# Performance work log

Measured on AMD Instinct MI355X. Metric: run time of the kernel, lower is better.

The kernel has to match this reference:

```python
import jax, jax.numpy as jnp
import numpy as np

DOF = 4
NUM_ITER = 10
Z_MIN = 0.1
EPS = 1e-5
MIN_LM_DIAG = 1e-6
MAX_LM_DIAG = 1e32
MIN_REL_DECREASE = 1e-3
INIT_RADIUS = 30.0
MAX_RADIUS = 1e16


def _proj_single(pose, x3d, K):
    # pose: (4,) [x, y, z, yaw]; x3d: (N,3); K: (3,3) -> (N,2)
    yaw = pose[3]
    s, c = jnp.sin(yaw), jnp.cos(yaw)
    z = jnp.zeros_like(c)
    o = jnp.ones_like(c)
    R = jnp.stack([jnp.stack([c, z, s]),
                   jnp.stack([z, o, z]),
                   jnp.stack([-s, z, c])])  # yaw_to_rot_mat
    p = x3d @ R.T + pose[:3]                 # (N,3) camera-frame points
    ph = p @ K.T                              # (N,3)
    zc = jnp.maximum(ph[:, 2:3], Z_MIN)       # depth clamp
    return ph[:, :2] / zc


def _res_single(pose, x3d, x2d, w2d, K):
    # weighted reprojection residual, flattened to (2N,)
    return ((_proj_single(pose, x3d, K) - x2d) * w2d).reshape(-1)


_res_b = jax.vmap(_res_single)
_jac_b = jax.vmap(jax.jacfwd(_res_single))  # (B, 2N, 4)


def _cost(r):
    return 0.5 * jnp.sum(r * r, axis=-1)


def lm_solve(x3d, x2d, w2d, pose_init, cam_mats):
    B = pose_init.shape[0]
    dt = pose_init.dtype
    pose = pose_init
    residual = _res_b(pose, x3d, x2d, w2d, cam_mats)
    jac = _jac_b(pose, x3d, x2d, w2d, cam_mats)
    cost = _cost(residual)
    radius = jnp.full((B,), INIT_RADIUS, dt)
    dec = jnp.full((B,), 2.0, dt)
    eye = jnp.eye(DOF, dtype=dt)

    def body(carry, _):
        pose, jac, residual, cost, radius, dec = carry
        jtj = jnp.einsum('bri,brj->bij', jac, jac)
        diag = jnp.clip(jnp.diagonal(jtj, axis1=-2, axis2=-1), MIN_LM_DIAG, MAX_LM_DIAG)
        jtj_lm = jtj + (diag / radius[:, None])[:, :, None] * eye  # LM damping
        grad = jnp.einsum('bri,br->bi', jac, residual)
        step = -jnp.linalg.solve(jtj_lm, grad[..., None])[..., 0]   # (B,4)
        pose_new = pose + step
        residual_new = _res_b(pose_new, x3d, x2d, w2d, cam_mats)
        cost_new = _cost(residual_new)
        jac_new = _jac_b(pose_new, x3d, x2d, w2d, cam_mats)
        # trust-region step acceptance (Ceres-style)
        model_cost_change = -jnp.einsum('bi,bi->b', step,
                                        grad + 0.5 * jnp.einsum('bij,bj->bi', jtj, step))
        rel = (cost - cost_new) / model_cost_change
        success = (rel >= MIN_REL_DECREASE) & (model_cost_change > 0.0)
        radius_s = jnp.minimum(radius / jnp.maximum(1.0 - (2.0 * rel - 1.0) ** 3, 1.0 / 3.0),
                               MAX_RADIUS)
        radius = jnp.where(success, radius_s, radius / dec)
        dec = jnp.where(success, 2.0, dec * 2.0)
        m = success[:, None]
        pose = jnp.where(m, pose_new, pose)
        residual = jnp.where(m, residual_new, residual)
        jac = jnp.where(success[:, None, None], jac_new, jac)
        cost = jnp.where(success, cost_new, cost)
        return (pose, jac, residual, cost, radius, dec), None

    (pose, jac, residual, cost, radius, dec), _ = jax.lax.scan(
        body, (pose, jac, residual, cost, radius, dec), None, length=NUM_ITER)
    return pose, cost


def gn_step(x3d, x2d, w2d, pose, cam_mats):
    residual = _res_b(pose, x3d, x2d, w2d, cam_mats)
    jac = _jac_b(pose, x3d, x2d, w2d, cam_mats)
    jtj = jnp.einsum('bri,brj->bij', jac, jac) + EPS * jnp.eye(DOF, dtype=pose.dtype)
    grad = jnp.einsum('bri,br->bi', jac, residual)
    return -jnp.linalg.solve(jtj, grad[..., None])[..., 0]


def setup_inputs() -> dict:
    key = jax.random.key(0)
    k1, k2, k3, k4, k5, k6 = jax.random.split(key, 6)
    B, N = 4096, 512
    x3d = jax.random.normal(k1, (B, N, 3), jnp.float32) * 0.5
    yaw_gt = jax.random.uniform(k2, (B, 1), jnp.float32, -0.5, 0.5)
    txy = jax.random.normal(k3, (B, 2), jnp.float32) * 0.2
    pose_gt = jnp.concatenate([txy, jnp.full((B, 1), 6.0, jnp.float32), yaw_gt], axis=-1)
    K = jnp.broadcast_to(jnp.array([[500.0, 0.0, 256.0],
                                    [0.0, 500.0, 256.0],
                                    [0.0, 0.0, 1.0]], jnp.float32), (B, 3, 3))
    x2d = jax.vmap(_proj_single)(pose_gt, x3d, K) + jax.random.normal(k4, (B, N, 2), jnp.float32) * 2.0
    w2d = jax.random.uniform(k5, (B, N, 2), jnp.float32) * 0.02
    noise = jax.random.normal(k6, (B, 4), jnp.float32) * jnp.array([0.2, 0.2, 0.5, 0.2], jnp.float32)
    pose_init = pose_gt + noise
    return {'x3d': x3d, 'x2d': x2d, 'w2d': w2d, 'pose_init': pose_init, 'cam_mats': K}


def reference(x3d, x2d, w2d, pose_init, cam_mats):
    # LMSolver.forward with with_pose_opt_plus=True, with_cost=True
    pose_opt, cost = lm_solve(x3d, x2d, w2d, pose_init, cam_mats)
    pose_opt_plus = pose_opt + gn_step(x3d, x2d, w2d, pose_opt, cam_mats)
    return pose_opt, cost, pose_opt_plus
```

## Files before the change

kernel.cpp:

```cpp
#include <hip/hip_runtime.h>
#include <math.h>

#define NUM_ITER 10
#define Z_MIN 0.1f

typedef float v2f __attribute__((ext_vector_type(2)));

__device__ inline float uniform_f(float v) {
    return __int_as_float(__builtin_amdgcn_readfirstlane(__float_as_int(v)));
}

__device__ inline float fast_rcp(float x) {
    return __builtin_amdgcn_rcpf(x);
}

__device__ inline v2f fma2(v2f a, v2f b, v2f c) {
#if __has_builtin(__builtin_elementwise_fma)
    return __builtin_elementwise_fma(a, b, c);
#else
    v2f r; r.x = fmaf(a.x, b.x, c.x); r.y = fmaf(a.y, b.y, c.y); return r;
#endif
}

__device__ inline v2f max2(v2f a, v2f b) {
#if __has_builtin(__builtin_elementwise_max)
    return __builtin_elementwise_max(a, b);
#else
    v2f r; r.x = fmaxf(a.x, b.x); r.y = fmaxf(a.y, b.y); return r;
#endif
}

template <int M>
__device__ inline void wave_reduce_uniform(float (&a)[M]) {
#pragma unroll
    for (int k = 0; k < M; ++k) {
        int t = __builtin_amdgcn_update_dpp(0, __float_as_int(a[k]), 0x121, 0xf, 0xf, true);
        a[k] += __int_as_float(t);
    }
#pragma unroll
    for (int k = 0; k < M; ++k) {
        int t = __builtin_amdgcn_update_dpp(0, __float_as_int(a[k]), 0x122, 0xf, 0xf, true);
        a[k] += __int_as_float(t);
    }
#pragma unroll
    for (int k = 0; k < M; ++k) {
        int t = __builtin_amdgcn_update_dpp(0, __float_as_int(a[k]), 0x124, 0xf, 0xf, true);
        a[k] += __int_as_float(t);
    }
#pragma unroll
    for (int k = 0; k < M; ++k) {
        int t = __builtin_amdgcn_update_dpp(0, __float_as_int(a[k]), 0x128, 0xf, 0xf, true);
        a[k] += __int_as_float(t);
    }
#pragma unroll
    for (int k = 0; k < M; ++k) {
        int t = __builtin_amdgcn_update_dpp(0, __float_as_int(a[k]), 0x142, 0xf, 0xf, true);
        a[k] += __int_as_float(t);
    }
#pragma unroll
    for (int k = 0; k < M; ++k) {
        int t = __builtin_amdgcn_update_dpp(0, __float_as_int(a[k]), 0x143, 0xf, 0xf, true);
        a[k] += __int_as_float(t);
    }
#pragma unroll
    for (int k = 0; k < M; ++k) {
        a[k] = __int_as_float(__builtin_amdgcn_readlane(__float_as_int(a[k]), 63));
    }
}

__device__ inline void solve4_spd(const float t[10], const float b[4], float x[4]) {
    const float d0 = t[0];
    const float i0 = fast_rcp(d0);
    const float L10 = t[1] * i0, L20 = t[2] * i0, L30 = t[3] * i0;
    const float d1 = t[4] - L10 * t[1];
    const float i1 = fast_rcp(d1);
    const float L21 = (t[5] - L20 * t[1]) * i1;
    const float L31 = (t[6] - L30 * t[1]) * i1;
    const float d2 = t[7] - L20 * t[2] - L21 * L21 * d1;
    const float i2 = fast_rcp(d2);
    const float L32 = (t[8] - L30 * t[2] - L31 * L21 * d1) * i2;
    const float d3 = t[9] - L30 * t[3] - L31 * L31 * d1 - L32 * L32 * d2;
    const float i3 = fast_rcp(d3);
    const float y0 = b[0];
    const float y1 = b[1] - L10 * y0;
    const float y2 = b[2] - L20 * y0 - L21 * y1;
    const float y3 = b[3] - L30 * y0 - L31 * y1 - L32 * y2;
    const float z0 = y0 * i0, z1 = y1 * i1, z2 = y2 * i2, z3 = y3 * i3;
    x[3] = z3;
    x[2] = z2 - L32 * z3;
    x[1] = z1 - L21 * x[2] - L31 * x[3];
    x[0] = z0 - L10 * x[1] - L20 * x[2] - L30 * x[3];
}

template <int PPL, bool EXACT>
__global__ __launch_bounds__(256) void lm_kernel(
    const float* __restrict__ x3d, const float* __restrict__ x2d,
    const float* __restrict__ w2d, const float* __restrict__ pose_init,
    const float* __restrict__ K, float* __restrict__ out, int B, int N)
{
    static_assert(PPL % 2 == 0, "PPL must be even");
    constexpr int NP = PPL / 2;

    const int wave = threadIdx.x >> 6;
    const int lane = threadIdx.x & 63;
    const int item = blockIdx.x * 4 + wave;
    if (item >= B) return;

    const float* Kb = K + (size_t)item * 9;
    const float K00 = uniform_f(Kb[0]), K01 = uniform_f(Kb[1]), K02 = uniform_f(Kb[2]);
    const float K10 = uniform_f(Kb[3]), K11 = uniform_f(Kb[4]), K12 = uniform_f(Kb[5]);
    const float K20 = uniform_f(Kb[6]), K21 = uniform_f(Kb[7]), K22 = uniform_f(Kb[8]);
    const bool spec = (K01 == 0.f) && (K10 == 0.f) && (K20 == 0.f) &&
                      (K21 == 0.f) && (K22 == 1.f);
    const float cxfx = K02 * fast_rcp(K00);
    const float cyfy = K12 * fast_rcp(K11);

    v2f X2[NP], Y2[NP], Z2[NP], Au2[NP], Av2[NP], Bu2[NP], Bv2[NP];
    if (EXACT) {
        const float4* p3 = reinterpret_cast<const float4*>(x3d + (size_t)item * N * 3) + lane * (3 * PPL / 4);
        const float4* p2 = reinterpret_cast<const float4*>(x2d + (size_t)item * N * 2) + lane * (2 * PPL / 4);
        const float4* pw = reinterpret_cast<const float4*>(w2d + (size_t)item * N * 2) + lane * (2 * PPL / 4);
        float f3[3 * PPL];
#pragma unroll
        for (int i = 0; i < 3 * PPL / 4; ++i) {
            const float4 t = p3[i];
            f3[4 * i] = t.x; f3[4 * i + 1] = t.y; f3[4 * i + 2] = t.z; f3[4 * i + 3] = t.w;
        }
#pragma unroll
        for (int j = 0; j < NP; ++j) {
            X2[j].x = f3[6 * j];     X2[j].y = f3[6 * j + 3];
            Y2[j].x = f3[6 * j + 1]; Y2[j].y = f3[6 * j + 4];
            Z2[j].x = f3[6 * j + 2]; Z2[j].y = f3[6 * j + 5];
        }
#pragma unroll
        for (int j = 0; j < NP; ++j) {
            const float4 tw = pw[j];
            const float4 to = p2[j];
            if (spec) {
                Au2[j].x = tw.x * K00;          Au2[j].y = tw.z * K00;
                Av2[j].x = tw.y * K11;          Av2[j].y = tw.w * K11;
                Bu2[j].x = tw.x * (K02 - to.x); Bu2[j].y = tw.z * (K02 - to.z);
                Bv2[j].x = tw.y * (K12 - to.y); Bv2[j].y = tw.w * (K12 - to.w);
            } else {
                Au2[j].x = tw.x;         Au2[j].y = tw.z;
                Av2[j].x = tw.y;         Av2[j].y = tw.w;
                Bu2[j].x = -tw.x * to.x; Bu2[j].y = -tw.z * to.z;
                Bv2[j].x = -tw.y * to.y; Bv2[j].y = -tw.w * to.w;
            }
        }
    } else {
        const float* x3b = x3d + (size_t)item * N * 3;
        const float* x2b = x2d + (size_t)item * N * 2;
        const float* w2b = w2d + (size_t)item * N * 2;
#pragma unroll
        for (int j = 0; j < NP; ++j) {
#pragma unroll
            for (int h = 0; h < 2; ++h) {
                const int p = lane + (2 * j + h) * 64;
                float X = 0.f, Y = 0.f, Z = 0.f, au = 0.f, av = 0.f, bu = 0.f, bv = 0.f;
                if (p < N) {
                    X = x3b[3 * p]; Y = x3b[3 * p + 1]; Z = x3b[3 * p + 2];
                    const float wu = w2b[2 * p], wv = w2b[2 * p + 1];
                    const float uo = x2b[2 * p], vo = x2b[2 * p + 1];
                    if (spec) {
                        au = wu * K00;        av = wv * K11;
                        bu = wu * (K02 - uo); bv = wv * (K12 - vo);
                    } else {
                        au = wu;       av = wv;
                        bu = -wu * uo; bv = -wv * vo;
                    }
                }
                if (h == 0) { X2[j].x = X; Y2[j].x = Y; Z2[j].x = Z;
                              Au2[j].x = au; Av2[j].x = av; Bu2[j].x = bu; Bv2[j].x = bv; }
                else        { X2[j].y = X; Y2[j].y = Y; Z2[j].y = Z;
                              Au2[j].y = au; Av2[j].y = av; Bu2[j].y = bu; Bv2[j].y = bv; }
            }
        }
    }

    float JtJ[10], grad[4];
    float cost = 0.f, radius = 30.0f, dec = 2.0f, mcc = 0.f;
#pragma unroll
    for (int k = 0; k < 10; ++k) JtJ[k] = 0.f;
#pragma unroll
    for (int k = 0; k < 4; ++k) grad[k] = 0.f;

    float ax = pose_init[(size_t)item * 4 + 0];
    float ay = pose_init[(size_t)item * 4 + 1];
    float az = pose_init[(size_t)item * 4 + 2];
    float ayaw = pose_init[(size_t)item * 4 + 3];
    float ex = ax, ey = ay, ez = az, eyaw = ayaw;
    float sn = __sinf(eyaw), cs = __cosf(eyaw);

#pragma clang loop unroll(disable)
    for (int it = 0; it <= NUM_ITER; ++it) {
        float acc[15];

        if (spec) {
            v2f s2[14];
#pragma unroll
            for (int k = 0; k < 14; ++k) s2[k] = (v2f)(0.f);
            const v2f cs2 = (v2f)(cs),  sn2 = (v2f)(sn);
            const v2f ex2 = (v2f)(ex),  ey2 = (v2f)(ey), ez2 = (v2f)(ez);
            const v2f zm2 = (v2f)(Z_MIN);
#pragma unroll
            for (int j = 0; j < NP; ++j) {
                const v2f X = X2[j], Y = Y2[j], Z = Z2[j];
                const v2f px = fma2(cs2, X, fma2(sn2, Z, ex2));
                const v2f py = Y + ey2;
                const v2f pz = fma2(-sn2, X, fma2(cs2, Z, ez2));
                const v2f zc = max2(pz, zm2);
                v2f inv; inv.x = fast_rcp(zc.x); inv.y = fast_rcp(zc.y);
                const v2f alpha = px * inv;
                const v2f beta  = py * inv;
                v2f t, tv;
                t.x  = (pz.x > Z_MIN) ? -alpha.x : cxfx;
                t.y  = (pz.y > Z_MIN) ? -alpha.y : cxfx;
                tv.x = (pz.x > Z_MIN) ? -beta.x  : cyfy;
                tv.y = (pz.y > Z_MIN) ? -beta.y  : cyfy;
                const v2f ru  = fma2(Au2[j], alpha, Bu2[j]);
                const v2f rv  = fma2(Av2[j], beta,  Bv2[j]);
                const v2f Ju0 = Au2[j] * inv;
                const v2f Jv1 = Av2[j] * inv;
                const v2f Ju2 = Ju0 * t;
                const v2f Jv2 = Jv1 * tv;
                const v2f a  = pz - ez2;
                const v2f bb = ex2 - px;
                const v2f q  = fma2(t, bb, a);
                const v2f Ju3 = Ju0 * q;
                const v2f Jv3 = Jv2 * bb;
                s2[0]  = fma2(Ju0, Ju0, s2[0]);
                s2[1]  = fma2(Ju0, Ju2, s2[1]);
                s2[2]  = fma2(Ju0, Ju3, s2[2]);
                s2[3]  = fma2(Jv1, Jv1, s2[3]);
                s2[4]  = fma2(Jv1, Jv2, s2[4]);
                s2[5]  = fma2(Jv1, Jv3, s2[5]);
                s2[6]  = fma2(Ju2, Ju2, fma2(Jv2, Jv2, s2[6]));
                s2[7]  = fma2(Ju2, Ju3, fma2(Jv2, Jv3, s2[7]));
                s2[8]  = fma2(Ju3, Ju3, fma2(Jv3, Jv3, s2[8]));
                s2[9]  = fma2(Ju0, ru, s2[9]);
                s2[10] = fma2(Jv1, rv, s2[10]);
                s2[11] = fma2(Ju2, ru, fma2(Jv2, rv, s2[11]));
                s2[12] = fma2(Ju3, ru, fma2(Jv3, rv, s2[12]));
                s2[13] = fma2(ru, ru, fma2(rv, rv, s2[13]));
            }
            float s[14];
#pragma unroll
            for (int k = 0; k < 14; ++k) s[k] = s2[k].x + s2[k].y;
            wave_reduce_uniform<14>(s);
            acc[0] = s[0];  acc[1] = 0.f;  acc[2] = s[1];  acc[3] = s[2];
            acc[4] = s[3];  acc[5] = s[4]; acc[6] = s[5];  acc[7] = s[6];
            acc[8] = s[7];  acc[9] = s[8];
            acc[10] = s[9]; acc[11] = s[10]; acc[12] = s[11]; acc[13] = s[12];
            acc[14] = s[13];
        } else {
#pragma unroll
            for (int k = 0; k < 15; ++k) acc[k] = 0.f;
#pragma unroll
            for (int j = 0; j < NP; ++j) {
#pragma unroll
                for (int h = 0; h < 2; ++h) {
                    const float X = h ? X2[j].y : X2[j].x;
                    const float Y = h ? Y2[j].y : Y2[j].x;
                    const float Z = h ? Z2[j].y : Z2[j].x;
                    const float au = h ? Au2[j].y : Au2[j].x;
                    const float av = h ? Av2[j].y : Av2[j].x;
                    const float bu = h ? Bu2[j].y : Bu2[j].x;
                    const float bv = h ? Bv2[j].y : Bv2[j].x;
                    const float px = fmaf(cs, X, fmaf(sn, Z, ex));
                    const float py = Y + ey;
                    const float pz = fmaf(-sn, X, fmaf(cs, Z, ez));
                    const float nu = fmaf(K00, px, fmaf(K01, py, K02 * pz));
                    const float nv = fmaf(K10, px, fmaf(K11, py, K12 * pz));
                    const float w  = fmaf(K20, px, fmaf(K21, py, K22 * pz));
                    const float zc  = fmaxf(w, Z_MIN);
                    const float inv = fast_rcp(zc);
                    const float gu = au * inv, gv = av * inv;
                    const float ru = fmaf(nu, gu, bu);
                    const float rv = fmaf(nv, gv, bv);
                    const float u = nu * inv, v = nv * inv;
                    const float fl  = (w > Z_MIN) ? 1.f : 0.f;
                    const float ufl = u * fl, vfl = v * fl;
                    const float a  = pz - ez;
                    const float bb = ex - px;
                    const float dnu3 = fmaf(K00, a, K02 * bb);
                    const float dnv3 = fmaf(K10, a, K12 * bb);
                    const float dw3  = fmaf(K20, a, K22 * bb);
                    float Ju[4], Jv[4];
                    Ju[0] = gu * fmaf(-ufl, K20, K00);  Jv[0] = gv * fmaf(-vfl, K20, K10);
                    Ju[1] = gu * fmaf(-ufl, K21, K01);  Jv[1] = gv * fmaf(-vfl, K21, K11);
                    Ju[2] = gu * fmaf(-ufl, K22, K02);  Jv[2] = gv * fmaf(-vfl, K22, K12);
                    Ju[3] = gu * fmaf(-ufl, dw3, dnu3); Jv[3] = gv * fmaf(-vfl, dw3, dnv3);
                    int idx = 0;
#pragma unroll
                    for (int r = 0; r < 4; ++r)
#pragma unroll
                        for (int c = r; c < 4; ++c) {
                            acc[idx] = fmaf(Ju[r], Ju[c], fmaf(Jv[r], Jv[c], acc[idx]));
                            ++idx;
                        }
#pragma unroll
                    for (int r = 0; r < 4; ++r)
                        acc[10 + r] = fmaf(Ju[r], ru, fmaf(Jv[r], rv, acc[10 + r]));
                    acc[14] = fmaf(ru, ru, fmaf(rv, rv, acc[14]));
                }
            }
            wave_reduce_uniform<15>(acc);
        }

        const float costN = 0.5f * acc[14];

        bool accept;
        if (it == 0) {
            accept = true;
        } else {
            const float rel = (cost - costN) * fast_rcp(mcc);
            const bool success = (rel >= 1e-3f) && (mcc > 0.0f);
            if (success) {
                const float q = 2.0f * rel - 1.0f;
                const float denom = fmaxf(1.0f - q * q * q, 1.0f / 3.0f);
                radius = fminf(radius * fast_rcp(denom), 1e16f);
                dec = 2.0f;
            } else {
                radius = radius * fast_rcp(dec);
                dec = dec * 2.0f;
            }
            accept = success;
        }
        if (accept) {
#pragma unroll
            for (int k = 0; k < 10; ++k) JtJ[k] = acc[k];
#pragma unroll
            for (int k = 0; k < 4; ++k) grad[k] = acc[10 + k];
            cost = costN;
            if (it > 0) { ax = ex; ay = ey; az = ez; ayaw = eyaw; }
        }

        if (it < NUM_ITER) {
            float A[10], rhs[4], stf[4];
#pragma unroll
            for (int k = 0; k < 10; ++k) A[k] = JtJ[k];
            const float irad = fast_rcp(radius);
            const float e0 = fminf(fmaxf(JtJ[0], 1e-6f), 1e32f) * irad;
            const float e1 = fminf(fmaxf(JtJ[4], 1e-6f), 1e32f) * irad;
            const float e2 = fminf(fmaxf(JtJ[7], 1e-6f), 1e32f) * irad;
            const float e3 = fminf(fmaxf(JtJ[9], 1e-6f), 1e32f) * irad;
            A[0] += e0; A[4] += e1; A[7] += e2; A[9] += e3;
#pragma unroll
            for (int r = 0; r < 4; ++r) rhs[r] = -grad[r];
            solve4_spd(A, rhs, stf);
            ex = ax + stf[0]; ey = ay + stf[1]; ez = az + stf[2]; eyaw = ayaw + stf[3];
            const float s0 = stf[0], s1 = stf[1], s2 = stf[2], s3 = stf[3];
            const float sg = s0 * grad[0] + s1 * grad[1] + s2 * grad[2] + s3 * grad[3];
            float sd = e0 * s0 * s0;
            sd = fmaf(e1 * s1, s1, sd);
            sd = fmaf(e2 * s2, s2, sd);
            sd = fmaf(e3 * s3, s3, sd);
            mcc = 0.5f * (sd - sg);
            sn = __sinf(eyaw); cs = __cosf(eyaw);
        } else if (lane == 0) {
            float* out_pose = out;
            float* out_cost = out + (size_t)B * 4;
            float* out_plus = out + (size_t)B * 5;
            out_pose[(size_t)item * 4 + 0] = ax;
            out_pose[(size_t)item * 4 + 1] = ay;
            out_pose[(size_t)item * 4 + 2] = az;
            out_pose[(size_t)item * 4 + 3] = ayaw;
            out_cost[item] = cost;
            float A[10], rhs[4], stf[4];
#pragma unroll
            for (int k = 0; k < 10; ++k) A[k] = JtJ[k];
            A[0] += 1e-5f; A[4] += 1e-5f; A[7] += 1e-5f; A[9] += 1e-5f;
#pragma unroll
            for (int r = 0; r < 4; ++r) rhs[r] = -grad[r];
            solve4_spd(A, rhs, stf);
            out_plus[(size_t)item * 4 + 0] = ax + stf[0];
            out_plus[(size_t)item * 4 + 1] = ay + stf[1];
            out_plus[(size_t)item * 4 + 2] = az + stf[2];
            out_plus[(size_t)item * 4 + 3] = ayaw + stf[3];
        }
    }
}

extern "C" void kernel_launch(void* const* d_in, const int* in_sizes, int n_in,
                              void* d_out, int out_size, void* d_ws, size_t ws_size,
                              hipStream_t stream) {
    const float* x3d       = (const float*)d_in[0];
    const float* x2d       = (const float*)d_in[1];
    const float* w2d       = (const float*)d_in[2];
    const float* pose_init = (const float*)d_in[3];
    const float* cam       = (const float*)d_in[4];
    float* out = (float*)d_out;

    const int B = in_sizes[3] / 4;
    const int N = in_sizes[0] / (3 * B);
    const int grid = (B + 3) / 4;

    if (N == 512) {
        lm_kernel<8, true><<<grid, 256, 0, stream>>>(x3d, x2d, w2d, pose_init, cam, out, B, N);
    } else if (N == 256) {
        lm_kernel<4, true><<<grid, 256, 0, stream>>>(x3d, x2d, w2d, pose_init, cam, out, B, N);
    } else if (N <= 128) {
        lm_kernel<2, false><<<grid, 256, 0, stream>>>(x3d, x2d, w2d, pose_init, cam, out, B, N);
    } else if (N <= 256) {
        lm_kernel<4, false><<<grid, 256, 0, stream>>>(x3d, x2d, w2d, pose_init, cam, out, B, N);
    } else if (N <= 512) {
        lm_kernel<8, false><<<grid, 256, 0, stream>>>(x3d, x2d, w2d, pose_init, cam, out, B, N);
    } else {
        lm_kernel<16, false><<<grid, 256, 0, stream>>>(x3d, x2d, w2d, pose_init, cam, out, B, N);
    }
}
```

Before: 125.8 us.

## Split each batch item across two waves with shared-memory cross-wave reduction

Each LM problem is now handled by two wavefronts instead of one. Each wave processes half of the points and combines its partial JtJ, gradient and cost sums with the other wave through shared memory, using a parity double-buffer and __syncthreads each iteration. This halves the per-lane point work and register footprint and doubles the number of waves, which targets the latency of the serial per-item iteration chain. In exchange it adds block-wide barriers and LDS traffic, duplicates the scalar solve in both waves, and doubles the grid size.

```diff
diff --git a/kernel.cpp b/kernel.cpp
--- a/kernel.cpp
+++ b/kernel.cpp
@@ -92,19 +92,21 @@
     x[0] = z0 - L10 * x[1] - L20 * x[2] - L30 * x[3];
 }
 
-template <int PPL, bool EXACT>
-__global__ __launch_bounds__(256) void lm_kernel(
+template <int NP, bool EXACT>
+__global__ __launch_bounds__(256) void lm_kernel2(
     const float* __restrict__ x3d, const float* __restrict__ x2d,
     const float* __restrict__ w2d, const float* __restrict__ pose_init,
     const float* __restrict__ K, float* __restrict__ out, int B, int N)
 {
-    static_assert(PPL % 2 == 0, "PPL must be even");
-    constexpr int NP = PPL / 2;
-
     const int wave = threadIdx.x >> 6;
     const int lane = threadIdx.x & 63;
-    const int item = blockIdx.x * 4 + wave;
-    if (item >= B) return;
+    const int ib   = wave >> 1;
+    const int wh   = wave & 1;
+    int item = blockIdx.x * 2 + ib;
+    const bool valid = (item < B);
+    if (!valid) item = B - 1;
+
+    __shared__ float red[2][2][2][15];
 
     const float* Kb = K + (size_t)item * 9;
     const float K00 = uniform_f(Kb[0]), K01 = uniform_f(Kb[1]), K02 = uniform_f(Kb[2]);
@@ -117,12 +119,15 @@
 
     v2f X2[NP], Y2[NP], Z2[NP], Au2[NP], Av2[NP], Bu2[NP], Bv2[NP];
     if (EXACT) {
-        const float4* p3 = reinterpret_cast<const float4*>(x3d + (size_t)item * N * 3) + lane * (3 * PPL / 4);
-        const float4* p2 = reinterpret_cast<const float4*>(x2d + (size_t)item * N * 2) + lane * (2 * PPL / 4);
-        const float4* pw = reinterpret_cast<const float4*>(w2d + (size_t)item * N * 2) + lane * (2 * PPL / 4);
-        float f3[3 * PPL];
-#pragma unroll
-        for (int i = 0; i < 3 * PPL / 4; ++i) {
+        const float4* p3 = reinterpret_cast<const float4*>(x3d + (size_t)item * N * 3)
+                           + wh * (3 * NP * 32) + lane * (6 * NP / 4);
+        const float4* p2 = reinterpret_cast<const float4*>(x2d + (size_t)item * N * 2)
+                           + wh * (2 * NP * 32) + lane * NP;
+        const float4* pw = reinterpret_cast<const float4*>(w2d + (size_t)item * N * 2)
+                           + wh * (2 * NP * 32) + lane * NP;
+        float f3[6 * NP];
+#pragma unroll
+        for (int i = 0; i < 6 * NP / 4; ++i) {
             const float4 t = p3[i];
             f3[4 * i] = t.x; f3[4 * i + 1] = t.y; f3[4 * i + 2] = t.z; f3[4 * i + 3] = t.w;
         }
@@ -156,7 +161,7 @@
         for (int j = 0; j < NP; ++j) {
 #pragma unroll
             for (int h = 0; h < 2; ++h) {
-                const int p = lane + (2 * j + h) * 64;
+                const int p = wh * (NP * 128) + (2 * j + h) * 64 + lane;
                 float X = 0.f, Y = 0.f, Z = 0.f, au = 0.f, av = 0.f, bu = 0.f, bv = 0.f;
                 if (p < N) {
                     X = x3b[3 * p]; Y = x3b[3 * p + 1]; Z = x3b[3 * p + 2];
@@ -195,6 +200,7 @@
 #pragma clang loop unroll(disable)
     for (int it = 0; it <= NUM_ITER; ++it) {
         float acc[15];
+        const int par = it & 1;
 
         if (spec) {
             v2f s2[14];
@@ -248,6 +254,13 @@
 #pragma unroll
             for (int k = 0; k < 14; ++k) s[k] = s2[k].x + s2[k].y;
             wave_reduce_uniform<14>(s);
+            if (lane == 0) {
+#pragma unroll
+                for (int k = 0; k < 14; ++k) red[ib][par][wh][k] = s[k];
+            }
+            __syncthreads();
+#pragma unroll
+            for (int k = 0; k < 14; ++k) s[k] += red[ib][par][wh ^ 1][k];
             acc[0] = s[0];  acc[1] = 0.f;  acc[2] = s[1];  acc[3] = s[2];
             acc[4] = s[3];  acc[5] = s[4]; acc[6] = s[5];  acc[7] = s[6];
             acc[8] = s[7];  acc[9] = s[8];
@@ -306,6 +319,13 @@
                 }
             }
             wave_reduce_uniform<15>(acc);
+            if (lane == 0) {
+#pragma unroll
+                for (int k = 0; k < 15; ++k) red[ib][par][wh][k] = acc[k];
+            }
+            __syncthreads();
+#pragma unroll
+            for (int k = 0; k < 15; ++k) acc[k] += red[ib][par][wh ^ 1][k];
         }
 
         const float costN = 0.5f * acc[14];
@@ -358,7 +378,7 @@
             sd = fmaf(e3 * s3, s3, sd);
             mcc = 0.5f * (sd - sg);
             sn = __sinf(eyaw); cs = __cosf(eyaw);
-        } else if (lane == 0) {
+        } else if (valid && wh == 0 && lane == 0) {
             float* out_pose = out;
             float* out_cost = out + (size_t)B * 4;
             float* out_plus = out + (size_t)B * 5;
@@ -394,19 +414,17 @@
 
     const int B = in_sizes[3] / 4;
     const int N = in_sizes[0] / (3 * B);
-    const int grid = (B + 3) / 4;
+    const int grid = (B + 1) / 2;
 
     if (N == 512) {
-        lm_kernel<8, true><<<grid, 256, 0, stream>>>(x3d, x2d, w2d, pose_init, cam, out, B, N);
-    } else if (N == 256) {
-        lm_kernel<4, true><<<grid, 256, 0, stream>>>(x3d, x2d, w2d, pose_init, cam, out, B, N);
-    } else if (N <= 128) {
-        lm_kernel<2, false><<<grid, 256, 0, stream>>>(x3d, x2d, w2d, pose_init, cam, out, B, N);
+        lm_kernel2<2, true><<<grid, 256, 0, stream>>>(x3d, x2d, w2d, pose_init, cam, out, B, N);
     } else if (N <= 256) {
-        lm_kernel<4, false><<<grid, 256, 0, stream>>>(x3d, x2d, w2d, pose_init, cam, out, B, N);
+        lm_kernel2<1, false><<<grid, 256, 0, stream>>>(x3d, x2d, w2d, pose_init, cam, out, B, N);
     } else if (N <= 512) {
-        lm_kernel<8, false><<<grid, 256, 0, stream>>>(x3d, x2d, w2d, pose_init, cam, out, B, N);
+        lm_kernel2<2, false><<<grid, 256, 0, stream>>>(x3d, x2d, w2d, pose_init, cam, out, B, N);
+    } else if (N <= 1024) {
+        lm_kernel2<4, false><<<grid, 256, 0, stream>>>(x3d, x2d, w2d, pose_init, cam, out, B, N);
     } else {
-        lm_kernel<16, false><<<grid, 256, 0, stream>>>(x3d, x2d, w2d, pose_init, cam, out, B, N);
-    }
-}
+        lm_kernel2<8, false><<<grid, 256, 0, stream>>>(x3d, x2d, w2d, pose_init, cam, out, B, N);
+    }
+}
```

Result: slower. 142.7 us (+13.4%).
